# Kernel tuning notes

Hardware: AMD Instinct MI355X
Metric: run time of the kernel (lower is better)

## Reference

```python
import jax, jax.numpy as jnp
import numpy as np

VAR_NUM = 96
EMBED_TIME = 128
INPUT_DIM = VAR_NUM * 2 + EMBED_TIME  # 320
ATTN_DIM = 64
N_HEADS = 8
ALL_DIM = ATTN_DIM * N_HEADS  # 512
B, N = 8, 2048
NEG_INF = -1e9  # finite stand-in for masked_fill(-inf); safe under softmax


def setup_inputs() -> dict:
    key = jax.random.key(0)
    ks = jax.random.split(key, 16)
    s = lambda d: 1.0 / np.sqrt(d)
    return {
        "times_in": jax.random.uniform(ks[0], (B, N), jnp.float32),
        "data_in": jax.random.normal(ks[1], (B, N, VAR_NUM), jnp.float32),
        "mask_in": jnp.ones((B, N, VAR_NUM), jnp.float32),
        "exist_times": jax.random.randint(ks[2], (B, N), 0, 2, jnp.int32),
        # TimeEmbedding params
        "w_per": jax.random.normal(ks[3], (1, EMBED_TIME - 1), jnp.float32),
        "b_per": jnp.zeros((EMBED_TIME - 1,), jnp.float32),
        "w_lin": jax.random.normal(ks[4], (1, 1), jnp.float32),
        "b_lin": jnp.zeros((1,), jnp.float32),
        # Attention params
        "Wq": jax.random.normal(ks[5], (INPUT_DIM, ALL_DIM), jnp.float32) * s(INPUT_DIM),
        "bq": jnp.zeros((ALL_DIM,), jnp.float32),
        "Wk": jax.random.normal(ks[6], (INPUT_DIM, ALL_DIM), jnp.float32) * s(INPUT_DIM),
        "bk": jnp.zeros((ALL_DIM,), jnp.float32),
        "Wv": jax.random.normal(ks[7], (INPUT_DIM, ALL_DIM), jnp.float32) * s(INPUT_DIM),
        "bv": jnp.zeros((ALL_DIM,), jnp.float32),
        "Wfc": jax.random.normal(ks[8], (ALL_DIM, ATTN_DIM), jnp.float32) * s(ALL_DIM),
        "bfc": jnp.zeros((ATTN_DIM,), jnp.float32),
    }


def reference(times_in, data_in, mask_in, exist_times,
              w_per, b_per, w_lin, b_lin,
              Wq, bq, Wk, bk, Wv, bv, Wfc, bfc):
    b, n = times_in.shape
    tt = times_in[..., None]  # [b, n, 1]
    # TimeEmbedding: [linear(tt), sin(periodic(tt))]
    te = jnp.concatenate([tt @ w_lin + b_lin, jnp.sin(tt @ w_per + b_per)], axis=-1)
    x = jnp.concatenate([data_in, mask_in, te], axis=-1)  # [b, n, INPUT_DIM]

    def heads(w, bias):
        return (x @ w + bias).reshape(b, n, N_HEADS, ATTN_DIM).transpose(0, 2, 1, 3)

    q, k, v = heads(Wq, bq), heads(Wk, bk), heads(Wv, bv)  # [b, h, n, d]
    # NOTE: custom scale uses sqrt(input_dim), not sqrt(head_dim)
    scores = jnp.einsum("bhqd,bhkd->bhqk", q, k) / jnp.sqrt(jnp.float32(INPUT_DIM))
    m = (exist_times != 0)
    scores = jnp.where(m[:, None, None, :], scores, NEG_INF)  # mask keys
    attn = jax.nn.softmax(scores, axis=-1)  # dropout p=0 in eval reference
    out = jnp.einsum("bhqk,bhkd->bhqd", attn, v)
    out = jnp.where(m[:, None, :, None], out, 0.0)  # zero masked query rows
    out = out.transpose(0, 2, 1, 3).reshape(b, n, ALL_DIM)
    return out @ Wfc + bfc  # [b, n, ATTN_DIM]
```

## Files before the change

kernel.cpp:

```cpp
#include <hip/hip_runtime.h>

#define N_ 2048
#define BN 16384
#define IN_DIM 320
#define QKV_N 1536
#define ALPHA 0.08064911f

typedef float f32x4 __attribute__((ext_vector_type(4)));
typedef short v8s __attribute__((ext_vector_type(8)));
typedef unsigned int u32x2 __attribute__((ext_vector_type(2)));

__device__ __forceinline__ short f2b(float f) {
  unsigned u = __builtin_bit_cast(unsigned, f);
  u = u + 0x7fff + ((u >> 16) & 1);
  return (short)(u >> 16);
}

__device__ __forceinline__ int piperm(int t) {
  return ((t >> 5) & 1) * 32 + ((t >> 2) & 3) * 8 + ((t >> 4) & 1) * 4 + (t & 3);
}

__device__ __forceinline__ size_t fragaddr(int ti, int r, int k) {
  return (size_t)ti * 512 + ((k >> 3) & 3) * 128 + r * 8 + (k & 7);
}

__global__ void scan_mask(const int* __restrict__ exist, int* __restrict__ prefix,
                          int* __restrict__ ntg, int* __restrict__ totals) {
  __shared__ int sums[256];
  int b = blockIdx.x;
  int t = threadIdx.x;
  const int* e = exist + b * 2048;
  int loc[8];
  int s = 0;
#pragma unroll
  for (int j = 0; j < 8; ++j) { loc[j] = s; s += (e[t * 8 + j] != 0) ? 1 : 0; }
  sums[t] = s;
  __syncthreads();
  for (int d = 1; d < 256; d <<= 1) {
    int v = (t >= d) ? sums[t - d] : 0;
    __syncthreads();
    sums[t] += v;
    __syncthreads();
  }
  int total = sums[255];
  int base = (t == 0) ? 0 : sums[t - 1];
#pragma unroll
  for (int j = 0; j < 8; ++j) prefix[b * 2048 + t * 8 + j] = base + loc[j];
  if (t == 0) { ntg[b] = (total + 63) >> 6; totals[b] = total; }
}

__global__ void build_x(const float* __restrict__ times, const float* __restrict__ data,
                        const float* __restrict__ maskv, const float* __restrict__ w_per,
                        const float* __restrict__ b_per, const float* __restrict__ w_lin,
                        const float* __restrict__ b_lin, const int* __restrict__ exist,
                        const int* __restrict__ prefix,
                        short* __restrict__ xF, short* __restrict__ xFc) {
  int row = blockIdx.x;
  int t = threadIdx.x;
  float tt = times[row];
  int rt = row >> 4, l16r = row & 15;
  int b = row >> 11;
  int dst = prefix[row];
  bool ex = exist[row] != 0;
  int tcb = (b * 128 + (dst >> 4)) * 10;
  int l16c = dst & 15;
  const float* dr = data + (size_t)row * 96;
  const float* mr = maskv + (size_t)row * 96;
  if (t < 96) {
    short v1 = f2b(dr[t]), v2 = f2b(mr[t]);
    int k2 = 96 + t;
    xF[fragaddr(rt * 10 + (t >> 5), l16r, t & 31)] = v1;
    xF[fragaddr(rt * 10 + (k2 >> 5), l16r, k2 & 31)] = v2;
    if (ex) {
      xFc[fragaddr(tcb + (t >> 5), l16c, t & 31)] = v1;
      xFc[fragaddr(tcb + (k2 >> 5), l16c, k2 & 31)] = v2;
    }
  }
  float val;
  if (t == 0) val = tt * w_lin[0] + b_lin[0];
  else        val = __sinf(tt * w_per[t - 1] + b_per[t - 1]);
  int k3 = 192 + t;
  short v3 = f2b(val);
  xF[fragaddr(rt * 10 + (k3 >> 5), l16r, k3 & 31)] = v3;
  if (ex) xFc[fragaddr(tcb + (k3 >> 5), l16c, k3 & 31)] = v3;
}

__global__ void transpose_w(const float* __restrict__ Wq, const float* __restrict__ Wk,
                            const float* __restrict__ Wv, const float* __restrict__ Wfc,
                            short* __restrict__ WtF, short* __restrict__ WfcT) {
  int idx = blockIdx.x * 256 + threadIdx.x;
  if (idx < QKV_N * IN_DIM) {
    int n = idx / IN_DIM, kk = idx - n * IN_DIM;
    const float* W = (n < 512) ? Wq : (n < 1024 ? Wk : Wv);
    WtF[fragaddr((n >> 4) * 10 + (kk >> 5), n & 15, kk & 31)] =
        f2b(W[(size_t)kk * 512 + (n & 511)]);
  } else {
    int j = idx - QKV_N * IN_DIM;
    int d = j >> 9, kk = j & 511;
    WfcT[j] = f2b(Wfc[kk * 64 + d]);
  }
}

__launch_bounds__(256)
__global__ void qkv_gemm(const short* __restrict__ xF, const short* __restrict__ xFc,
                         const short* __restrict__ WtF,
                         const float* __restrict__ bq, const float* __restrict__ bk,
                         const float* __restrict__ bv, const int* __restrict__ totals,
                         short* __restrict__ q, short* __restrict__ kc, short* __restrict__ vc) {
  int bm = blockIdx.x;
  int bn = blockIdx.y;
  int w = bn >> 2;
  int bb = bm >> 4, bq16 = bm & 15;
  if (w != 0 && bq16 * 128 >= totals[bb]) return;
  int tid = threadIdx.x, wave = tid >> 6, lane = tid & 63;
  int wm = wave >> 1, wn = wave & 1;
  int l16 = lane & 15, lh = lane >> 4;
  int voff = lane * 8;
  const short* ap = (w == 0) ? xF + (size_t)(bm * 8 + wm * 4) * 10 * 512
                             : xFc + (size_t)(bb * 128 + bq16 * 8 + wm * 4) * 10 * 512;
  const short* bp = WtF + (size_t)(bn * 8 + wn * 4) * 10 * 512;
  f32x4 acc[4][4] = {};
  v8s af[4], bfr[4];
#pragma unroll
  for (int m = 0; m < 4; ++m) af[m] = *(const v8s*)&ap[(size_t)(m * 10) * 512 + voff];
#pragma unroll
  for (int n = 0; n < 4; ++n) bfr[n] = *(const v8s*)&bp[(size_t)(n * 10) * 512 + voff];
#pragma unroll 1
  for (int kt = 0; kt < 10; ++kt) {
#pragma unroll
    for (int m = 0; m < 4; ++m)
#pragma unroll
      for (int n = 0; n < 4; ++n)
        acc[m][n] = __builtin_amdgcn_mfma_f32_16x16x32_bf16(af[m], bfr[n], acc[m][n], 0, 0, 0);
    if (kt < 9) {
#pragma unroll
      for (int m = 0; m < 4; ++m) af[m] = *(const v8s*)&ap[(size_t)(m * 10 + kt + 1) * 512 + voff];
#pragma unroll
      for (int n = 0; n < 4; ++n) bfr[n] = *(const v8s*)&bp[(size_t)(n * 10 + kt + 1) * 512 + voff];
    }
  }
  if (w == 0) {
#pragma unroll
    for (int m = 0; m < 4; ++m) {
      int row0 = bm * 128 + wm * 64 + m * 16 + lh * 4;
#pragma unroll
      for (int n = 0; n < 4; ++n) {
        int c = (bn * 128 + wn * 64 + n * 16 + l16) & 511;
        float bb2 = bq[c];
        int h = c >> 6, d = c & 63;
#pragma unroll
        for (int r = 0; r < 4; ++r) {
          int rr = row0 + r;
          int b = rr >> 11, ntok = rr & 2047;
          q[(((size_t)(b * 8 + h) * N_ + ntok) << 6) + d] = f2b((acc[m][n][r] + bb2) * ALPHA);
        }
      }
    }
  } else {
    short* dbuf = (w == 1) ? kc : vc;
    const float* bias = (w == 1) ? bk : bv;
#pragma unroll
    for (int m = 0; m < 4; ++m) {
      int crow0 = bq16 * 128 + wm * 64 + m * 16 + lh * 4;
#pragma unroll
      for (int n = 0; n < 4; ++n) {
        int c = ((bn & 3) * 128 + wn * 64 + n * 16 + l16);
        float bb2 = bias[c];
        int h = c >> 6, d = c & 63;
#pragma unroll
        for (int r = 0; r < 4; ++r)
          dbuf[(((size_t)(bb * 8 + h) * N_ + crow0 + r) << 6) + d] = f2b(acc[m][n][r] + bb2);
      }
    }
  }
}

__launch_bounds__(256)
__global__ void fragmentize(short* __restrict__ kc, short* __restrict__ vc,
                            const int* __restrict__ ntg, const int* __restrict__ totals) {
  __shared__ short Ks[64][66];
  __shared__ short Vs[64][66];
  int bh = blockIdx.x;
  int b = bh >> 3;
  int nt = ntg[b], total = totals[b];
  int tid = threadIdx.x;
  size_t hb = (size_t)bh * N_ * 64;
  for (int tile = blockIdx.y; tile < nt; tile += 8) {
    int base = tile * 64;
#pragma unroll
    for (int s = 0; s < 2; ++s) {
      int c = tid + s * 256, r = c >> 3, c8 = c & 7;
      v8s kv = {0, 0, 0, 0, 0, 0, 0, 0};
      v8s vv = {0, 0, 0, 0, 0, 0, 0, 0};
      if (base + r < total) {
        kv = *(const v8s*)&kc[hb + (size_t)(base + r) * 64 + c8 * 8];
        vv = *(const v8s*)&vc[hb + (size_t)(base + r) * 64 + c8 * 8];
      }
      *(v8s*)&Ks[r][c8 * 8] = kv;
      *(v8s*)&Vs[r][c8 * 8] = vv;
    }
    __syncthreads();
#pragma unroll
    for (int s = 0; s < 2; ++s) {
      int c = tid + s * 256;
      int i = c >> 6, lh2 = (c >> 4) & 3, r16 = c & 15;
      *(v8s*)&kc[hb + (size_t)tile * 4096 + c * 8] =
          *(const v8s*)&Ks[(i >> 1) * 16 + r16][(i & 1) * 32 + lh2 * 8];
      int l16 = c & 15, lh = (c >> 4) & 3, kc2 = (c >> 6) & 1, n2 = c >> 7;
      int d = n2 * 16 + l16;
      v8s o;
#pragma unroll
      for (int jj = 0; jj < 8; ++jj) {
        int t2 = kc2 * 32 + (jj >> 2) * 16 + lh * 4 + (jj & 3);
        o[jj] = Vs[t2][d];
      }
      *(v8s*)&vc[hb + (size_t)tile * 4096 + c * 8] = o;
    }
    __syncthreads();
  }
}

__launch_bounds__(256, 2)
__global__ void attn_kernel(const short* __restrict__ q, const short* __restrict__ kT,
                            const short* __restrict__ vT, const int* __restrict__ ntg,
                            const int* __restrict__ totals, const int* __restrict__ exist,
                            short* __restrict__ att) {
  int bx = blockIdx.x;
  int bh = ((bx >> 6) << 3) | (bx & 7);
  int qblk = (bx >> 3) & 7;
  int b = bh >> 3, h = bh & 7;
  int tid = threadIdx.x, wave = tid >> 6, lane = tid & 63;
  int l16 = lane & 15, lh = lane >> 4;
  int q0 = qblk * 256 + wave * 64;
  int nt = ntg[b];
  float padf = (float)(nt * 64 - totals[b]);
  const short* qp = q + (size_t)bh * N_ * 64;
  const short* kpt = kT + (size_t)bh * 131072;
  const short* vpt = vT + (size_t)bh * 131072;
  const int* ex = exist + b * N_;
  v8s qf[4][2];
#pragma unroll
  for (int m = 0; m < 4; ++m)
#pragma unroll
    for (int kcx = 0; kcx < 2; ++kcx)
      qf[m][kcx] = *(const v8s*)&qp[(size_t)(q0 + m * 16 + l16) * 64 + kcx * 32 + lh * 8];
  f32x4 oacc[4][4] = {};
  f32x4 lacc[4] = {};
  const f32x4 zf = {0.f, 0.f, 0.f, 0.f};
  v8s ones;
#pragma unroll
  for (int j = 0; j < 8; ++j) ones[j] = (short)0x3F80;
  int voff = lane * 8;
  v8s kf[8], vf[8];
#pragma unroll
  for (int i = 0; i < 8; ++i) {
    kf[i] = *(const v8s*)&kpt[i * 512 + voff];
    vf[i] = *(const v8s*)&vpt[i * 512 + voff];
  }
#pragma unroll 1
  for (int kt = 0; kt < nt; ++kt) {
    const short* kn = kpt + (size_t)(kt + 1) * 4096;
    const short* vn = vpt + (size_t)(kt + 1) * 4096;
    bool pre = (kt + 1 < nt);
#pragma unroll
    for (int mh = 0; mh < 2; ++mh) {
      f32x4 sacc[2][4];
#pragma unroll
      for (int n = 0; n < 4; ++n)
#pragma unroll
        for (int mm = 0; mm < 2; ++mm) {
          sacc[mm][n] = __builtin_amdgcn_mfma_f32_16x16x32_bf16(kf[n * 2], qf[mh * 2 + mm][0], zf, 0, 0, 0);
          sacc[mm][n] = __builtin_amdgcn_mfma_f32_16x16x32_bf16(kf[n * 2 + 1], qf[mh * 2 + mm][1], sacc[mm][n], 0, 0, 0);
        }
      if (mh == 1 && pre)
#pragma unroll
        for (int i = 0; i < 8; ++i) kf[i] = *(const v8s*)&kn[i * 512 + voff];
      v8s pf[2][2];
#pragma unroll
      for (int mm = 0; mm < 2; ++mm)
#pragma unroll
        for (int kcx = 0; kcx < 2; ++kcx)
#pragma unroll
          for (int half = 0; half < 2; ++half) {
            int n = kcx * 2 + half;
            float p0 = __builtin_amdgcn_exp2f(sacc[mm][n][0]);
            float p1 = __builtin_amdgcn_exp2f(sacc[mm][n][1]);
            float p2 = __builtin_amdgcn_exp2f(sacc[mm][n][2]);
            float p3 = __builtin_amdgcn_exp2f(sacc[mm][n][3]);
            uint w0, w1;
            asm("v_cvt_pk_bf16_f32 %0, %1, %2" : "=v"(w0) : "v"(p0), "v"(p1));
            asm("v_cvt_pk_bf16_f32 %0, %1, %2" : "=v"(w1) : "v"(p2), "v"(p3));
            ((uint*)&pf[mm][kcx])[half * 2]     = w0;
            ((uint*)&pf[mm][kcx])[half * 2 + 1] = w1;
          }
#pragma unroll
      for (int kcx = 0; kcx < 2; ++kcx) {
#pragma unroll
        for (int mm = 0; mm < 2; ++mm)
          lacc[mh * 2 + mm] = __builtin_amdgcn_mfma_f32_16x16x32_bf16(pf[mm][kcx], ones, lacc[mh * 2 + mm], 0, 0, 0);
#pragma unroll
        for (int n = 0; n < 4; ++n)
#pragma unroll
          for (int mm = 0; mm < 2; ++mm)
            oacc[mh * 2 + mm][n] = __builtin_amdgcn_mfma_f32_16x16x32_bf16(pf[mm][kcx], vf[n * 2 + kcx], oacc[mh * 2 + mm][n], 0, 0, 0);
      }
    }
    if (pre) {
#pragma unroll
      for (int i = 0; i < 8; ++i) vf[i] = *(const v8s*)&vn[i * 512 + voff];
    }
  }
#pragma unroll
  for (int m = 0; m < 4; ++m)
#pragma unroll
    for (int r = 0; r < 4; ++r) {
      int row = q0 + m * 16 + lh * 4 + r;
      float qm = (ex[row] != 0) ? 1.f : 0.f;
      float inv = qm / fmaxf(lacc[m][r] - padf, 1e-20f);
#pragma unroll
      for (int n = 0; n < 4; ++n)
        att[((size_t)(b * N_ + row)) * 512 + h * 64 + n * 16 + l16] = f2b(oacc[m][n][r] * inv);
    }
}

__launch_bounds__(256)
__global__ void out_gemm(const short* __restrict__ att, const short* __restrict__ WfcT,
                         const float* __restrict__ bfc, float* __restrict__ out) {
  __shared__ short As[128][40];
  __shared__ short Bs[64][40];
  int bm = blockIdx.x;
  int tid = threadIdx.x, wave = tid >> 6, lane = tid & 63;
  int l16 = lane & 15, lh = lane >> 4;
  f32x4 acc[2][4] = {};
  for (int kt = 0; kt < 16; ++kt) {
    int k0 = kt * 32;
#pragma unroll
    for (int s = 0; s < 2; ++s) {
      int c = tid + s * 256;
      int r = c >> 2, c8 = c & 3;
      *(v8s*)&As[r][c8 * 8] = *(const v8s*)&att[(size_t)(bm * 128 + r) * 512 + k0 + c8 * 8];
    }
    { int r = tid >> 2, c8 = tid & 3;
      if (r < 64) *(v8s*)&Bs[r][c8 * 8] = *(const v8s*)&WfcT[(size_t)r * 512 + k0 + c8 * 8]; }
    __syncthreads();
    v8s bfr[4];
#pragma unroll
    for (int n = 0; n < 4; ++n) bfr[n] = *(const v8s*)&Bs[n * 16 + l16][lh * 8];
#pragma unroll
    for (int m = 0; m < 2; ++m) {
      v8s af = *(const v8s*)&As[wave * 32 + m * 16 + l16][lh * 8];
#pragma unroll
      for (int n = 0; n < 4; ++n)
        acc[m][n] = __builtin_amdgcn_mfma_f32_16x16x32_bf16(af, bfr[n], acc[m][n], 0, 0, 0);
    }
    __syncthreads();
  }
#pragma unroll
  for (int m = 0; m < 2; ++m)
#pragma unroll
    for (int n = 0; n < 4; ++n) {
      float bb = bfc[n * 16 + l16];
#pragma unroll
      for (int r = 0; r < 4; ++r) {
        int row = bm * 128 + wave * 32 + m * 16 + lh * 4 + r;
        out[(size_t)row * 64 + n * 16 + l16] = acc[m][n][r] + bb;
      }
    }
}

extern "C" void kernel_launch(void* const* d_in, const int* in_sizes, int n_in,
                              void* d_out, int out_size, void* d_ws, size_t ws_size,
                              hipStream_t stream) {
  const float* times = (const float*)d_in[0];
  const float* data  = (const float*)d_in[1];
  const float* maskv = (const float*)d_in[2];
  const int*   exist = (const int*)d_in[3];
  const float* w_per = (const float*)d_in[4];
  const float* b_per = (const float*)d_in[5];
  const float* w_lin = (const float*)d_in[6];
  const float* b_lin = (const float*)d_in[7];
  const float* Wq  = (const float*)d_in[8];
  const float* bq  = (const float*)d_in[9];
  const float* Wk  = (const float*)d_in[10];
  const float* bk  = (const float*)d_in[11];
  const float* Wv  = (const float*)d_in[12];
  const float* bv  = (const float*)d_in[13];
  const float* Wfc = (const float*)d_in[14];
  const float* bfc = (const float*)d_in[15];
  float* out = (float*)d_out;

  char* ws = (char*)d_ws;
  short* xF    = (short*)(ws);
  short* WtF   = (short*)(ws + 10485760);
  short* WfcT  = (short*)(ws + 11468800);
  short* qb    = (short*)(ws + 11534336);
  short* kcb   = (short*)(ws + 28311552);
  short* vcb   = (short*)(ws + 45088768);
  short* att   = (short*)(ws + 61865984);
  short* xFc   = (short*)(ws + 61865984);
  int*   prefix= (int*)(ws + 78675968);
  int*   ntg   = (int*)(ws + 78741504);
  int*   totals= (int*)(ws + 78741536);

  scan_mask<<<8, 256, 0, stream>>>(exist, prefix, ntg, totals);
  build_x<<<BN, 128, 0, stream>>>(times, data, maskv, w_per, b_per, w_lin, b_lin,
                                  exist, prefix, xF, xFc);
  transpose_w<<<2048, 256, 0, stream>>>(Wq, Wk, Wv, Wfc, WtF, WfcT);
  qkv_gemm<<<dim3(128, 12), 256, 0, stream>>>(xF, xFc, WtF, bq, bk, bv, totals, qb, kcb, vcb);
  fragmentize<<<dim3(64, 8), 256, 0, stream>>>(kcb, vcb, ntg, totals);
  attn_kernel<<<512, 256, 0, stream>>>(qb, kcb, vcb, ntg, totals, exist, att);
  out_gemm<<<128, 256, 0, stream>>>(att, WfcT, bfc, out);
}
```

Measured before the change: 109.6 us.

## Stage build_x tiles in LDS and compact rows with a separate gather kernel

build_x now processes 16-row tiles per block, staging bf16 values in shared memory and writing the fragment layout with 16-byte vector stores instead of scattered 2-byte stores. The compacted key/value input is no longer written inside build_x. It is produced by a new compact_x kernel that gathers rows through a source-row index computed in scan_mask. This targets uncoalesced scattered stores in the input preparation. In exchange it adds one extra kernel launch and a re-read of xF.

```diff
diff --git a/kernel.cpp b/kernel.cpp
--- a/kernel.cpp
+++ b/kernel.cpp
@@ -16,16 +16,13 @@
   return (short)(u >> 16);
 }
 
-__device__ __forceinline__ int piperm(int t) {
-  return ((t >> 5) & 1) * 32 + ((t >> 2) & 3) * 8 + ((t >> 4) & 1) * 4 + (t & 3);
-}
-
 __device__ __forceinline__ size_t fragaddr(int ti, int r, int k) {
   return (size_t)ti * 512 + ((k >> 3) & 3) * 128 + r * 8 + (k & 7);
 }
 
 __global__ void scan_mask(const int* __restrict__ exist, int* __restrict__ prefix,
-                          int* __restrict__ ntg, int* __restrict__ totals) {
+                          int* __restrict__ ntg, int* __restrict__ totals,
+                          int* __restrict__ srcrow) {
   __shared__ int sums[256];
   int b = blockIdx.x;
   int t = threadIdx.x;
@@ -45,44 +42,67 @@
   int total = sums[255];
   int base = (t == 0) ? 0 : sums[t - 1];
 #pragma unroll
-  for (int j = 0; j < 8; ++j) prefix[b * 2048 + t * 8 + j] = base + loc[j];
+  for (int j = 0; j < 8; ++j) {
+    int row = t * 8 + j;
+    int dst = base + loc[j];
+    prefix[b * 2048 + row] = dst;
+    if (e[row] != 0) srcrow[b * 2048 + dst] = row;
+  }
   if (t == 0) { ntg[b] = (total + 63) >> 6; totals[b] = total; }
 }
 
 __global__ void build_x(const float* __restrict__ times, const float* __restrict__ data,
                         const float* __restrict__ maskv, const float* __restrict__ w_per,
                         const float* __restrict__ b_per, const float* __restrict__ w_lin,
-                        const float* __restrict__ b_lin, const int* __restrict__ exist,
-                        const int* __restrict__ prefix,
-                        short* __restrict__ xF, short* __restrict__ xFc) {
-  int row = blockIdx.x;
+                        const float* __restrict__ b_lin, short* __restrict__ xF) {
+  __shared__ short Ls[16][328];
+  int rt = blockIdx.x;
   int t = threadIdx.x;
+  int r = t >> 4, seg = t & 15;
+  int row = rt * 16 + r;
   float tt = times[row];
-  int rt = row >> 4, l16r = row & 15;
-  int b = row >> 11;
-  int dst = prefix[row];
-  bool ex = exist[row] != 0;
-  int tcb = (b * 128 + (dst >> 4)) * 10;
-  int l16c = dst & 15;
   const float* dr = data + (size_t)row * 96;
   const float* mr = maskv + (size_t)row * 96;
-  if (t < 96) {
-    short v1 = f2b(dr[t]), v2 = f2b(mr[t]);
-    int k2 = 96 + t;
-    xF[fragaddr(rt * 10 + (t >> 5), l16r, t & 31)] = v1;
-    xF[fragaddr(rt * 10 + (k2 >> 5), l16r, k2 & 31)] = v2;
-    if (ex) {
-      xFc[fragaddr(tcb + (t >> 5), l16c, t & 31)] = v1;
-      xFc[fragaddr(tcb + (k2 >> 5), l16c, k2 & 31)] = v2;
-    }
-  }
-  float val;
-  if (t == 0) val = tt * w_lin[0] + b_lin[0];
-  else        val = __sinf(tt * w_per[t - 1] + b_per[t - 1]);
-  int k3 = 192 + t;
-  short v3 = f2b(val);
-  xF[fragaddr(rt * 10 + (k3 >> 5), l16r, k3 & 31)] = v3;
-  if (ex) xFc[fragaddr(tcb + (k3 >> 5), l16c, k3 & 31)] = v3;
+#pragma unroll
+  for (int j = 0; j < 20; ++j) {
+    int col = seg * 20 + j;
+    float val;
+    if (col < 96) val = dr[col];
+    else if (col < 192) val = mr[col - 96];
+    else {
+      int k = col - 192;
+      val = (k == 0) ? (tt * w_lin[0] + b_lin[0]) : __sinf(tt * w_per[k - 1] + b_per[k - 1]);
+    }
+    Ls[r][col] = f2b(val);
+  }
+  __syncthreads();
+  short* dst = xF + (size_t)rt * 5120;
+  for (int c = t; c < 640; c += 256) {
+    int ti = c >> 6, rem = c & 63, kq = rem >> 4, rr = rem & 15;
+    v8s o;
+#pragma unroll
+    for (int j = 0; j < 8; ++j) o[j] = Ls[rr][ti * 32 + kq * 8 + j];
+    *(v8s*)&dst[c * 8] = o;
+  }
+}
+
+__global__ void compact_x(const short* __restrict__ xF, const int* __restrict__ srcrow,
+                          const int* __restrict__ totals, short* __restrict__ xFc) {
+  int b = blockIdx.y;
+  int ct = blockIdx.x;
+  int total = totals[b];
+  if (ct * 16 >= total) return;
+  int t = threadIdx.x;
+  const int* sr = srcrow + b * 2048;
+  short* dst = xFc + (size_t)(b * 128 + ct) * 5120;
+  for (int c = t; c < 640; c += 256) {
+    int ti = c >> 6, rem = c & 63, kq = rem >> 4, rr = rem & 15;
+    int drow = ct * 16 + rr;
+    int src = (drow < total) ? sr[drow] : sr[0];
+    int grow = b * 2048 + src;
+    v8s o = *(const v8s*)&xF[(size_t)(grow >> 4) * 5120 + ti * 512 + kq * 128 + (grow & 15) * 8];
+    *(v8s*)&dst[c * 8] = o;
+  }
 }
 
 __global__ void transpose_w(const float* __restrict__ Wq, const float* __restrict__ Wk,
@@ -401,10 +421,11 @@
   int*   prefix= (int*)(ws + 78675968);
   int*   ntg   = (int*)(ws + 78741504);
   int*   totals= (int*)(ws + 78741536);
-
-  scan_mask<<<8, 256, 0, stream>>>(exist, prefix, ntg, totals);
-  build_x<<<BN, 128, 0, stream>>>(times, data, maskv, w_per, b_per, w_lin, b_lin,
-                                  exist, prefix, xF, xFc);
+  int*   srcrow= (int*)(ws + 78741568);
+
+  scan_mask<<<8, 256, 0, stream>>>(exist, prefix, ntg, totals, srcrow);
+  build_x<<<1024, 256, 0, stream>>>(times, data, maskv, w_per, b_per, w_lin, b_lin, xF);
+  compact_x<<<dim3(128, 8), 256, 0, stream>>>(xF, srcrow, totals, xFc);
   transpose_w<<<2048, 256, 0, stream>>>(Wq, Wk, Wv, Wfc, WtF, WfcT);
   qkv_gemm<<<dim3(128, 12), 256, 0, stream>>>(xF, xFc, WtF, bq, bk, bv, totals, qb, kcb, vcb);
   fragmentize<<<dim3(64, 8), 256, 0, stream>>>(kcb, vcb, ntg, totals);
```

Result: slower. 115.2 us (+5.1%).
